# Kernel optimization log

Hardware: AMD Instinct MI355X
Metric: run time of the kernel (lower is better)

Reference implementation:

```python
import jax, jax.numpy as jnp
import numpy as np

HIDDEN = 1024
HEADS = 16
HEAD_DIM = HIDDEN // HEADS

def setup_inputs() -> dict:
    key = jax.random.key(0)
    k1, k2, k3 = jax.random.split(key, 3)
    scale = 1.0 / np.sqrt(HIDDEN)
    return {
        "x": jax.random.normal(k1, (2, 2048, HIDDEN), dtype=jnp.float32),
        "w_qkv": jax.random.normal(k2, (HIDDEN, 3 * HIDDEN), dtype=jnp.float32) * scale,
        "b_qkv": jnp.zeros((3 * HIDDEN,), dtype=jnp.float32),
        "w_out": jax.random.normal(k3, (HIDDEN, HIDDEN), dtype=jnp.float32) * scale,
        "b_out": jnp.zeros((HIDDEN,), dtype=jnp.float32),
    }

def reference(x, w_qkv, b_qkv, w_out, b_out):
    B, S, H = x.shape
    qkv = x @ w_qkv + b_qkv                              # (B,S,3H)
    qkv = qkv.reshape(B, S, 3, HEADS, HEAD_DIM)
    qkv = jnp.transpose(qkv, (2, 0, 3, 1, 4))            # (3,B,nh,S,hd)
    q, k, v = qkv[0], qkv[1], qkv[2]
    scores = jnp.einsum("bhqd,bhkd->bhqk", q, k) / np.sqrt(HEAD_DIM)
    causal = jnp.triu(jnp.ones((S, S), dtype=bool), k=1)  # True above diagonal
    scores = jnp.where(causal, -jnp.inf, scores)
    attn = jax.nn.softmax(scores, axis=-1)               # dropout: eval mode (identity)
    out = jnp.einsum("bhqk,bhkd->bhqd", attn, v)
    out = jnp.transpose(out, (0, 2, 1, 3)).reshape(B, S, H)
    return out @ w_out + b_out
```

## Files before the change

### kernel.cpp

```cpp
#include <hip/hip_runtime.h>
#include <hip/hip_bf16.h>

typedef short short8 __attribute__((ext_vector_type(8)));
typedef float f32x4 __attribute__((ext_vector_type(4)));

typedef const __attribute__((address_space(1))) unsigned int* gas_ptr;
typedef __attribute__((address_space(3))) unsigned int* las_ptr;
#define ASYNC16(g, l) __builtin_amdgcn_global_load_lds((gas_ptr)(g), (las_ptr)(l), 16, 0, 0)

__device__ __forceinline__ unsigned short f2bf(float f) {
    unsigned int u = __builtin_bit_cast(unsigned int, f);
    u += 0x7fff + ((u >> 16) & 1);
    return (unsigned short)(u >> 16);
}

__device__ __forceinline__ unsigned int pkbf_trunc(float lo, float hi) {
    return __builtin_amdgcn_perm(__builtin_bit_cast(unsigned int, hi),
                                 __builtin_bit_cast(unsigned int, lo), 0x07060302u);
}

__global__ __launch_bounds__(256) void cast_f32_bf16(
    const float* __restrict__ in, unsigned short* __restrict__ out, int n)
{
    int i = (blockIdx.x * 256 + threadIdx.x) * 4;
    if (i >= n) return;
    float4 v = *(const float4*)(in + i);
    ushort4 o;
    o.x = f2bf(v.x); o.y = f2bf(v.y); o.z = f2bf(v.z); o.w = f2bf(v.w);
    *(ushort4*)(out + i) = o;
}

__global__ __launch_bounds__(256) void transpose_cast(
    const float* __restrict__ w, unsigned short* __restrict__ wt, int K, int N)
{
    __shared__ unsigned short tile[64 * 65];
    int k0 = blockIdx.y * 64, n0 = blockIdx.x * 64;
    for (int i = threadIdx.x; i < 64 * 64; i += 256) {
        int r = i >> 6, c = i & 63;
        tile[r * 65 + c] = f2bf(w[(size_t)(k0 + r) * N + n0 + c]);
    }
    __syncthreads();
    for (int i = threadIdx.x; i < 64 * 64; i += 256) {
        int r = i >> 6, c = i & 63;
        wt[(size_t)(n0 + r) * K + k0 + c] = tile[c * 65 + r];
    }
}


template<bool OUT_BF16, bool QKV>
__global__ __launch_bounds__(256, 3) void gemm_bt(
    const unsigned short* __restrict__ A,
    const unsigned short* __restrict__ Bt,
    const float* __restrict__ bias,
    void* __restrict__ C,
    unsigned short* __restrict__ vTp,
    int M, int N, int K)
{
    __shared__ __align__(16) unsigned short As[128 * 32];
    __shared__ __align__(16) unsigned short Bs[128 * 32];
    const int tid = threadIdx.x;
    const int lane = tid & 63;
    const int wave = tid >> 6;
    const int wr = wave >> 1, wc = wave & 1;
    const int m0 = blockIdx.x * 128, n0 = blockIdx.y * 128;
    const int fr = lane & 15, fq = lane >> 4;

    f32x4 acc[4][4] = {};

    const int grow = lane >> 2;
    const int gcol = (lane & 3) * 8;
    const unsigned short* Ag = A  + (size_t)(m0 + wave * 32 + grow) * K + gcol;
    const unsigned short* Bg = Bt + (size_t)(n0 + wave * 32 + grow) * K + gcol;
    unsigned short* AsW0 = As + (wave * 32) * 32;
    unsigned short* AsW1 = As + (wave * 32 + 16) * 32;
    unsigned short* BsW0 = Bs + (wave * 32) * 32;
    unsigned short* BsW1 = Bs + (wave * 32 + 16) * 32;

    for (int k0 = 0; k0 < K; k0 += 32) {
        __syncthreads();
        ASYNC16(Ag + k0,          AsW0);
        ASYNC16(Ag + 16 * K + k0, AsW1);
        ASYNC16(Bg + k0,          BsW0);
        ASYNC16(Bg + 16 * K + k0, BsW1);
        __syncthreads();

        short8 af[4], bfr[4];
#pragma unroll
        for (int i = 0; i < 4; i++)
            af[i] = *(const short8*)(As + (wr * 64 + i * 16 + fr) * 32 + fq * 8);
#pragma unroll
        for (int j = 0; j < 4; j++)
            bfr[j] = *(const short8*)(Bs + (wc * 64 + j * 16 + fr) * 32 + fq * 8);
#pragma unroll
        for (int i = 0; i < 4; i++)
#pragma unroll
            for (int j = 0; j < 4; j++)
                acc[i][j] = __builtin_amdgcn_mfma_f32_16x16x32_bf16(af[i], bfr[j], acc[i][j], 0, 0, 0);
    }

#pragma unroll
    for (int i = 0; i < 4; i++)
#pragma unroll
        for (int j = 0; j < 4; j++) {
            int col = n0 + wc * 64 + j * 16 + fr;
            float bv = bias[col];
            if (QKV && col >= 2048) {
                int hh = (col - 2048) >> 6, d = col & 63;
#pragma unroll
                for (int r = 0; r < 4; r++) {
                    int row = m0 + wr * 64 + i * 16 + fq * 4 + r;
                    int bb = row >> 11, s = row & 2047;
                    vTp[((size_t)(bb * 16 + hh) * 64 + d) * 2048 + s] = f2bf(acc[i][j][r] + bv);
                }
            } else {
#pragma unroll
                for (int r = 0; r < 4; r++) {
                    int row = m0 + wr * 64 + i * 16 + fq * 4 + r;
                    float v = acc[i][j][r] + bv;
                    if (OUT_BF16)
                        ((unsigned short*)C)[(size_t)row * N + col] = f2bf(v);
                    else
                        ((float*)C)[(size_t)row * N + col] = v;
                }
            }
        }
}


template<int RG0>
__device__ __forceinline__ void attn_step(
    const unsigned short* __restrict__ Ks0, const unsigned short* __restrict__ Ks1,
    const unsigned short* __restrict__ Vs0, const unsigned short* __restrict__ Vs1,
    unsigned short* __restrict__ Psw,
    const short8 (&qf)[2][2], const short8 ones,
    f32x4 (&o_acc)[2][4], f32x4 (&l_acc)[2],
    int j0, int fr, int fq,
    const int (&qrow0)[2], const bool (&diag)[2])
{
    f32x4 s[2][4];
#pragma unroll
    for (int rg = RG0; rg < 2; rg++)
#pragma unroll
        for (int t = 0; t < 4; t++)
            s[rg][t] = (f32x4){0.f, 0.f, 0.f, 0.f};

#pragma unroll
    for (int t = 0; t < 4; t++) {
        short8 kf0 = *(const short8*)(Ks0 + (t * 16 + fr) * 32 + fq * 8);
        short8 kf1 = *(const short8*)(Ks1 + (t * 16 + fr) * 32 + fq * 8);
#pragma unroll
        for (int rg = RG0; rg < 2; rg++) {
            s[rg][t] = __builtin_amdgcn_mfma_f32_16x16x32_bf16(qf[rg][0], kf0, s[rg][t], 0, 0, 0);
            s[rg][t] = __builtin_amdgcn_mfma_f32_16x16x32_bf16(qf[rg][1], kf1, s[rg][t], 0, 0, 0);
        }
    }

#pragma unroll
    for (int rg = RG0; rg < 2; rg++) {
        unsigned short* prow = Psw + rg * (16 * 72);
#pragma unroll
        for (int t = 0; t < 4; t++) {
            float p[4];
#pragma unroll
            for (int r = 0; r < 4; r++) {
                float v = __expf(s[rg][t][r] * 0.125f - 8.0f);
                if (diag[rg] && (j0 + t * 16 + fr) > (qrow0[rg] + fq * 4 + r)) v = 0.f;
                p[r] = v;
            }
            unsigned int pk01 = pkbf_trunc(p[0], p[1]);
            unsigned int pk23 = pkbf_trunc(p[2], p[3]);
            int base = (fq * 4) * 72 + t * 16 + fr;
            prow[base]       = (unsigned short)pk01;
            prow[base + 72]  = (unsigned short)(pk01 >> 16);
            prow[base + 144] = (unsigned short)pk23;
            prow[base + 216] = (unsigned short)(pk23 >> 16);
        }
    }

#pragma unroll
    for (int ks = 0; ks < 2; ks++) {
        const unsigned short* Vsb = ks ? Vs1 : Vs0;
        short8 pf[2];
#pragma unroll
        for (int rg = RG0; rg < 2; rg++)
            pf[rg] = *(const short8*)(Psw + rg * (16 * 72) + fr * 72 + ks * 32 + fq * 8);
#pragma unroll
        for (int t = 0; t < 4; t++) {
            short8 vf = *(const short8*)(Vsb + (t * 16 + fr) * 32 + fq * 8);
#pragma unroll
            for (int rg = RG0; rg < 2; rg++)
                o_acc[rg][t] = __builtin_amdgcn_mfma_f32_16x16x32_bf16(pf[rg], vf, o_acc[rg][t], 0, 0, 0);
        }
#pragma unroll
        for (int rg = RG0; rg < 2; rg++)
            l_acc[rg] = __builtin_amdgcn_mfma_f32_16x16x32_bf16(pf[rg], ones, l_acc[rg], 0, 0, 0);
    }
}

__global__ __launch_bounds__(256, 4) void flash_attn(
    const unsigned short* __restrict__ qkv,
    const unsigned short* __restrict__ vT,
    unsigned short* __restrict__ out)
{
    const int bx = blockIdx.x, h = blockIdx.y, b = blockIdx.z;
    const int qtA = bx, qtB = 31 - bx;
    const int tid = threadIdx.x, wave = tid >> 6, lane = tid & 63;
    const int fr = lane & 15, fq = lane >> 4;
    const size_t RS = 3072;

    const unsigned short* Qb = qkv + (size_t)b * 2048 * RS + h * 64;
    const unsigned short* Kb = Qb + 1024;
    const unsigned short* Vt = vT + (size_t)(b * 16 + h) * 64 * 2048;

    __shared__ __align__(16) unsigned short Ks[2][64 * 32];
    __shared__ __align__(16) unsigned short Vs[2][64 * 32];
    __shared__ __align__(16) unsigned short Ps[4][2 * 16 * 72];

    short8 qf[2][2];
    int qrow0[2];
#pragma unroll
    for (int rg = 0; rg < 2; rg++) {
        int qt = rg ? qtB : qtA;
        qrow0[rg] = qt * 64 + wave * 16;
        const unsigned short* qrow = Qb + (size_t)(qrow0[rg] + fr) * RS;
        qf[rg][0] = *(const short8*)(qrow + fq * 8);
        qf[rg][1] = *(const short8*)(qrow + 32 + fq * 8);
    }
    short8 ones;
#pragma unroll
    for (int e = 0; e < 8; e++) ones[e] = (short)0x3F80;

    f32x4 o_acc[2][4] = {};
    f32x4 l_acc[2] = {};

    const int grow = lane >> 2;
    const int gcol = (lane & 3) * 8;
    const unsigned short* Kg = Kb + (size_t)(wave * 16 + grow) * RS + gcol;
    const unsigned short* Vg = Vt + (size_t)(wave * 16 + grow) * 2048 + gcol;
    unsigned short* KsW0 = Ks[0] + (wave * 16) * 32;
    unsigned short* KsW1 = Ks[1] + (wave * 16) * 32;
    unsigned short* VsW0 = Vs[0] + (wave * 16) * 32;
    unsigned short* VsW1 = Vs[1] + (wave * 16) * 32;

    const int njt = qtB + 1;
    for (int jt = 0; jt < njt; jt++) {
        const int j0 = jt * 64;
        __syncthreads();
        ASYNC16(Kg + (size_t)j0 * RS,      KsW0);
        ASYNC16(Kg + (size_t)j0 * RS + 32, KsW1);
        ASYNC16(Vg + j0,      VsW0);
        ASYNC16(Vg + j0 + 32, VsW1);
        __syncthreads();

        bool diag[2] = { jt == qtA, jt == qtB };
        if (jt <= qtA)
            attn_step<0>(Ks[0], Ks[1], Vs[0], Vs[1], Ps[wave], qf, ones,
                         o_acc, l_acc, j0, fr, fq, qrow0, diag);
        else
            attn_step<1>(Ks[0], Ks[1], Vs[0], Vs[1], Ps[wave], qf, ones,
                         o_acc, l_acc, j0, fr, fq, qrow0, diag);
    }

#pragma unroll
    for (int rg = 0; rg < 2; rg++)
#pragma unroll
        for (int t = 0; t < 4; t++)
#pragma unroll
            for (int r = 0; r < 4; r++) {
                int row = qrow0[rg] + fq * 4 + r;
                out[(size_t)(b * 2048 + row) * 1024 + h * 64 + t * 16 + fr] =
                    f2bf(o_acc[rg][t][r] / l_acc[rg][r]);
            }
}

extern "C" void kernel_launch(void* const* d_in, const int* in_sizes, int n_in,
                              void* d_out, int out_size, void* d_ws, size_t ws_size,
                              hipStream_t stream) {
    const float* x      = (const float*)d_in[0];
    const float* w_qkv  = (const float*)d_in[1];
    const float* b_qkv  = (const float*)d_in[2];
    const float* w_out  = (const float*)d_in[3];
    const float* b_out  = (const float*)d_in[4];
    float* out = (float*)d_out;

    char* ws = (char*)d_ws;
    unsigned short* x_b    = (unsigned short*)(ws);
    unsigned short* wqkv_t = (unsigned short*)(ws + 8u  * 1024 * 1024);
    unsigned short* wout_t = (unsigned short*)(ws + 14u * 1024 * 1024);
    unsigned short* qkv    = (unsigned short*)(ws + 16u * 1024 * 1024);
    unsigned short* attn   = (unsigned short*)(ws + 40u * 1024 * 1024);
    unsigned short* vT     = (unsigned short*)(ws + 48u * 1024 * 1024);

    cast_f32_bf16<<<4096, 256, 0, stream>>>(x, x_b, 2 * 2048 * 1024);
    transpose_cast<<<dim3(48, 16), 256, 0, stream>>>(w_qkv, wqkv_t, 1024, 3072);
    transpose_cast<<<dim3(16, 16), 256, 0, stream>>>(w_out, wout_t, 1024, 1024);
    gemm_bt<true, true ><<<dim3(32, 24), 256, 0, stream>>>(x_b,  wqkv_t, b_qkv, qkv, vT, 4096, 3072, 1024);
    flash_attn<<<dim3(16, 16, 2), 256, 0, stream>>>(qkv, vT, attn);
    gemm_bt<false, false><<<dim3(32, 8),  256, 0, stream>>>(attn, wout_t, b_out, out, nullptr, 4096, 1024, 1024);
}
```

Baseline: 202.1 us.

## Split attention KV range across two blocks with partial-sum reduce kernel

The flash attention grid is doubled by splitting each query-pair's key range into two halves, each handled by a separate block that writes unnormalized partial outputs (bf16) and row sums. A new reduce kernel then adds the partials and normalizes. The QKV buffer now has a 2048-element row stride because V is written only transposed. The P tile in LDS drops its padding in favour of an XOR-like rotation swizzle. The intent is better occupancy and load balance on the many-CU GPU, at the cost of an extra launch, extra global traffic, and bf16 rounding of the partials.

```diff
diff --git a/kernel.cpp b/kernel.cpp
--- a/kernel.cpp
+++ b/kernel.cpp
@@ -13,7 +13,10 @@
     u += 0x7fff + ((u >> 16) & 1);
     return (unsigned short)(u >> 16);
 }
-
+__device__ __forceinline__ float bf2f(unsigned short s) {
+    unsigned int u = (unsigned int)s << 16;
+    return __builtin_bit_cast(float, u);
+}
 __device__ __forceinline__ unsigned int pkbf_trunc(float lo, float hi) {
     return __builtin_amdgcn_perm(__builtin_bit_cast(unsigned int, hi),
                                  __builtin_bit_cast(unsigned int, lo), 0x07060302u);
@@ -113,14 +116,15 @@
                     vTp[((size_t)(bb * 16 + hh) * 64 + d) * 2048 + s] = f2bf(acc[i][j][r] + bv);
                 }
             } else {
+                const int cstride = QKV ? 2048 : N;
 #pragma unroll
                 for (int r = 0; r < 4; r++) {
                     int row = m0 + wr * 64 + i * 16 + fq * 4 + r;
                     float v = acc[i][j][r] + bv;
                     if (OUT_BF16)
-                        ((unsigned short*)C)[(size_t)row * N + col] = f2bf(v);
+                        ((unsigned short*)C)[(size_t)row * cstride + col] = f2bf(v);
                     else
-                        ((float*)C)[(size_t)row * N + col] = v;
+                        ((float*)C)[(size_t)row * cstride + col] = v;
                 }
             }
         }
@@ -157,7 +161,7 @@
 
 #pragma unroll
     for (int rg = RG0; rg < 2; rg++) {
-        unsigned short* prow = Psw + rg * (16 * 72);
+        unsigned short* prow = Psw + rg * (16 * 64);
 #pragma unroll
         for (int t = 0; t < 4; t++) {
             float p[4];
@@ -169,11 +173,12 @@
             }
             unsigned int pk01 = pkbf_trunc(p[0], p[1]);
             unsigned int pk23 = pkbf_trunc(p[2], p[3]);
-            int base = (fq * 4) * 72 + t * 16 + fr;
+            int colp = (t * 16 + fr + 16 * fq) & 63;
+            int base = (fq * 4) * 64 + colp;
             prow[base]       = (unsigned short)pk01;
-            prow[base + 72]  = (unsigned short)(pk01 >> 16);
-            prow[base + 144] = (unsigned short)pk23;
-            prow[base + 216] = (unsigned short)(pk23 >> 16);
+            prow[base + 64]  = (unsigned short)(pk01 >> 16);
+            prow[base + 128] = (unsigned short)pk23;
+            prow[base + 192] = (unsigned short)(pk23 >> 16);
         }
     }
 
@@ -182,8 +187,10 @@
         const unsigned short* Vsb = ks ? Vs1 : Vs0;
         short8 pf[2];
 #pragma unroll
-        for (int rg = RG0; rg < 2; rg++)
-            pf[rg] = *(const short8*)(Psw + rg * (16 * 72) + fr * 72 + ks * 32 + fq * 8);
+        for (int rg = RG0; rg < 2; rg++) {
+            int colp = (ks * 32 + fq * 8 + 16 * ((fr >> 2) & 3)) & 63;
+            pf[rg] = *(const short8*)(Psw + rg * (16 * 64) + fr * 64 + colp);
+        }
 #pragma unroll
         for (int t = 0; t < 4; t++) {
             short8 vf = *(const short8*)(Vsb + (t * 16 + fr) * 32 + fq * 8);
@@ -200,13 +207,16 @@
 __global__ __launch_bounds__(256, 4) void flash_attn(
     const unsigned short* __restrict__ qkv,
     const unsigned short* __restrict__ vT,
-    unsigned short* __restrict__ out)
-{
-    const int bx = blockIdx.x, h = blockIdx.y, b = blockIdx.z;
-    const int qtA = bx, qtB = 31 - bx;
+    unsigned short* __restrict__ Opart,
+    float* __restrict__ lpart)
+{
+    const int p = blockIdx.x;
+    const int g = blockIdx.y;
+    const int h = blockIdx.z & 15, b = blockIdx.z >> 4;
+    const int qtA = p, qtB = 31 - p;
     const int tid = threadIdx.x, wave = tid >> 6, lane = tid & 63;
     const int fr = lane & 15, fq = lane >> 4;
-    const size_t RS = 3072;
+    const size_t RS = 2048;
 
     const unsigned short* Qb = qkv + (size_t)b * 2048 * RS + h * 64;
     const unsigned short* Kb = Qb + 1024;
@@ -214,7 +224,7 @@
 
     __shared__ __align__(16) unsigned short Ks[2][64 * 32];
     __shared__ __align__(16) unsigned short Vs[2][64 * 32];
-    __shared__ __align__(16) unsigned short Ps[4][2 * 16 * 72];
+    __shared__ __align__(16) unsigned short Ps[4][2 * 16 * 64];
 
     short8 qf[2][2];
     int qrow0[2];
@@ -242,8 +252,11 @@
     unsigned short* VsW0 = Vs[0] + (wave * 16) * 32;
     unsigned short* VsW1 = Vs[1] + (wave * 16) * 32;
 
-    const int njt = qtB + 1;
-    for (int jt = 0; jt < njt; jt++) {
+    const int mid = (p >= 8) ? 8 : (16 - p);
+    const int lo = g ? mid : 0;
+    const int hi = g ? (32 - p) : mid;
+
+    for (int jt = lo; jt < hi; jt++) {
         const int j0 = jt * 64;
         __syncthreads();
         ASYNC16(Kg + (size_t)j0 * RS,      KsW0);
@@ -261,16 +274,50 @@
                          o_acc, l_acc, j0, fr, fq, qrow0, diag);
     }
 
-#pragma unroll
-    for (int rg = 0; rg < 2; rg++)
+    unsigned short* Og = Opart + (size_t)g * 4096 * 1024;
+    float* lg = lpart + (size_t)g * 4096 * 16;
+#pragma unroll
+    for (int rg = 0; rg < 2; rg++) {
 #pragma unroll
         for (int t = 0; t < 4; t++)
 #pragma unroll
             for (int r = 0; r < 4; r++) {
                 int row = qrow0[rg] + fq * 4 + r;
-                out[(size_t)(b * 2048 + row) * 1024 + h * 64 + t * 16 + fr] =
-                    f2bf(o_acc[rg][t][r] / l_acc[rg][r]);
+                Og[(size_t)(b * 2048 + row) * 1024 + h * 64 + t * 16 + fr] = f2bf(o_acc[rg][t][r]);
             }
+        if (fr == 0) {
+#pragma unroll
+            for (int r = 0; r < 4; r++) {
+                int row = qrow0[rg] + fq * 4 + r;
+                lg[(size_t)(b * 2048 + row) * 16 + h] = l_acc[rg][r];
+            }
+        }
+    }
+}
+
+__global__ __launch_bounds__(256) void reduce_attn(
+    const unsigned short* __restrict__ Opart, const float* __restrict__ lpart,
+    unsigned short* __restrict__ out)
+{
+    int i = (blockIdx.x * 256 + threadIdx.x) * 8;
+    int row = i >> 10, h = (i & 1023) >> 6;
+    float lsum = lpart[(size_t)row * 16 + h] + lpart[(size_t)4096 * 16 + row * 16 + h];
+    float inv = 1.0f / lsum;
+    ushort4 a0 = *(const ushort4*)(Opart + i);
+    ushort4 a1 = *(const ushort4*)(Opart + i + 4);
+    ushort4 b0 = *(const ushort4*)(Opart + (size_t)4096 * 1024 + i);
+    ushort4 b1 = *(const ushort4*)(Opart + (size_t)4096 * 1024 + i + 4);
+    ushort4 o0, o1;
+    o0.x = f2bf((bf2f(a0.x) + bf2f(b0.x)) * inv);
+    o0.y = f2bf((bf2f(a0.y) + bf2f(b0.y)) * inv);
+    o0.z = f2bf((bf2f(a0.z) + bf2f(b0.z)) * inv);
+    o0.w = f2bf((bf2f(a0.w) + bf2f(b0.w)) * inv);
+    o1.x = f2bf((bf2f(a1.x) + bf2f(b1.x)) * inv);
+    o1.y = f2bf((bf2f(a1.y) + bf2f(b1.y)) * inv);
+    o1.z = f2bf((bf2f(a1.z) + bf2f(b1.z)) * inv);
+    o1.w = f2bf((bf2f(a1.w) + bf2f(b1.w)) * inv);
+    *(ushort4*)(out + i) = o0;
+    *(ushort4*)(out + i + 4) = o1;
 }
 
 extern "C" void kernel_launch(void* const* d_in, const int* in_sizes, int n_in,
@@ -288,13 +335,16 @@
     unsigned short* wqkv_t = (unsigned short*)(ws + 8u  * 1024 * 1024);
     unsigned short* wout_t = (unsigned short*)(ws + 14u * 1024 * 1024);
     unsigned short* qkv    = (unsigned short*)(ws + 16u * 1024 * 1024);
-    unsigned short* attn   = (unsigned short*)(ws + 40u * 1024 * 1024);
-    unsigned short* vT     = (unsigned short*)(ws + 48u * 1024 * 1024);
+    unsigned short* attn   = (unsigned short*)(ws + 32u * 1024 * 1024);
+    unsigned short* vT     = (unsigned short*)(ws + 40u * 1024 * 1024);
+    unsigned short* Opart  = (unsigned short*)(ws + 48u * 1024 * 1024);
+    float*          lpart  = (float*)         (ws + 64u * 1024 * 1024);
 
     cast_f32_bf16<<<4096, 256, 0, stream>>>(x, x_b, 2 * 2048 * 1024);
     transpose_cast<<<dim3(48, 16), 256, 0, stream>>>(w_qkv, wqkv_t, 1024, 3072);
     transpose_cast<<<dim3(16, 16), 256, 0, stream>>>(w_out, wout_t, 1024, 1024);
     gemm_bt<true, true ><<<dim3(32, 24), 256, 0, stream>>>(x_b,  wqkv_t, b_qkv, qkv, vT, 4096, 3072, 1024);
-    flash_attn<<<dim3(16, 16, 2), 256, 0, stream>>>(qkv, vT, attn);
+    flash_attn<<<dim3(16, 2, 32), 256, 0, stream>>>(qkv, vT, Opart, lpart);
+    reduce_attn<<<2048, 256, 0, stream>>>(Opart, lpart, attn);
     gemm_bt<false, false><<<dim3(32, 8),  256, 0, stream>>>(attn, wout_t, b_out, out, nullptr, 4096, 1024, 1024);
 }
```

After: 206.9 us. 1.02x slower.
